# Kernel tuning notes

Hardware: AMD Instinct MI355X
Metric: run time of the kernel (lower is better)

## Reference

```python
import jax, jax.numpy as jnp
import numpy as np

B, D, H, E = 32768, 128, 512, 16

def setup_inputs() -> dict:
    key = jax.random.key(0)
    ks = jax.random.split(key, 5)
    x = jax.random.normal(ks[0], (B, 1, D), dtype=jnp.float32)
    s1 = 1.0 / float(np.sqrt(H))   # init_ uses last-dim size: w1 last dim = H
    s2 = 1.0 / float(np.sqrt(D))   # w2 last dim = D
    sg = 1.0 / float(np.sqrt(D))   # nn.Linear(D, E) default init scale
    w1 = jax.random.uniform(ks[1], (E, D, H), minval=-s1, maxval=s1, dtype=jnp.float32)
    w2 = jax.random.uniform(ks[2], (E, H, D), minval=-s2, maxval=s2, dtype=jnp.float32)
    wg = jax.random.uniform(ks[3], (D, E), minval=-sg, maxval=sg, dtype=jnp.float32)
    bg = jax.random.uniform(ks[4], (E,), minval=-sg, maxval=sg, dtype=jnp.float32)
    return {"x": x, "w1": w1, "w2": w2, "wg": wg, "bg": bg}

def reference(x, w1, w2, wg, bg):
    xt = x[:, 0, :]                                   # (B, D); seq dim is 1 by construction
    logits = xt @ wg + bg                             # (B, E)
    topk_vals, topk_idx = jax.lax.top_k(logits, 1)    # (B, 1) each
    scores = jax.nn.softmax(topk_vals, axis=-1)       # (B, 1); all ones for k=1
    # every expert processes every token (faithful to the reference)
    hidden = jax.nn.gelu(jnp.einsum('bd,edh->ebh', xt, w1), approximate=False)  # (E, B, H)
    eout = jnp.einsum('ebh,ehd->ebd', hidden, w2)     # (E, B, D)
    # gather selected expert per token, scale, sum over k
    sel = jnp.take_along_axis(eout.transpose(1, 0, 2), topk_idx[:, :, None], axis=1)  # (B, 1, D)
    return (sel * scores[:, :, None]).sum(axis=1)     # (B, D)
```

## Files before the change

kernel.cpp:

```cpp
#include <hip/hip_runtime.h>
#include <hip/hip_bf16.h>
#include <math.h>

#define NB 32768
#define DD 128
#define HH 512
#define EE 16
#define TM 32
#define HC 64
#define NCH (HH / HC)

typedef __attribute__((ext_vector_type(8))) short short8;
typedef __attribute__((ext_vector_type(4))) float f32x4;
typedef __attribute__((address_space(1))) const unsigned short gc_us;
typedef __attribute__((address_space(3))) unsigned short lds_us;

__device__ __forceinline__ unsigned short f2bf(float f) {
  union { float f; unsigned u; } v; v.f = f;
  unsigned r = v.u + 0x7fffu + ((v.u >> 16) & 1u);
  return (unsigned short)(r >> 16);
}

__device__ __forceinline__ float fast_erf(float z) {
  float a = fabsf(z);
  float t = __builtin_amdgcn_rcpf(1.0f + 0.3275911f * a);
  float y = t * (0.254829592f + t * (-0.284496736f + t * (1.421413741f +
            t * (-1.453152027f + t * 1.061405429f))));
  float r = 1.0f - y * __expf(-a * a);
  return z < 0.0f ? -r : r;
}

__global__ __launch_bounds__(256) void prep_kernel(
    const float* __restrict__ x, const float* __restrict__ wg,
    const float* __restrict__ bg, const float* __restrict__ w1,
    const float* __restrict__ w2, int* __restrict__ counts,
    int* __restrict__ rows, unsigned short* __restrict__ w1T,
    unsigned short* __restrict__ w2T) {
  __shared__ __align__(16) char smem[50816];
  int tid = threadIdx.x;

  if (blockIdx.x >= 512) {
    float (*tile)[65] = (float (*)[65])smem;
    int tp = blockIdx.x - 512;
    const float* src; unsigned short* dst; int S, Sd;
    if (tp < 256) {
      int e = tp >> 4, t2 = tp & 15;
      int d0 = (t2 >> 3) * 64, h0 = (t2 & 7) * 64;
      src = w1 + (size_t)e * DD * HH + (size_t)d0 * HH + h0; S = HH;
      dst = w1T + (size_t)e * HH * DD + (size_t)h0 * DD + d0; Sd = DD;
    } else {
      int t = tp - 256;
      int e = t >> 4, t2 = t & 15;
      int h0 = (t2 >> 1) * 64, d0 = (t2 & 1) * 64;
      src = w2 + (size_t)e * HH * DD + (size_t)h0 * DD + d0; S = DD;
      dst = w2T + (size_t)e * DD * HH + (size_t)d0 * HH + h0; Sd = HH;
    }
    #pragma unroll
    for (int i = 0; i < 4; ++i) {
      int u = tid + i * 256, r = u >> 4, c = (u & 15) * 4;
      float4 v = *(const float4*)(src + (size_t)r * S + c);
      tile[r][c + 0] = v.x; tile[r][c + 1] = v.y;
      tile[r][c + 2] = v.z; tile[r][c + 3] = v.w;
    }
    __syncthreads();
    #pragma unroll
    for (int i = 0; i < 4; ++i) {
      int u = tid + i * 256, tr = u >> 4, tc = (u & 15) * 4;
      ushort4 p;
      p.x = f2bf(tile[tc + 0][tr]); p.y = f2bf(tile[tc + 1][tr]);
      p.z = f2bf(tile[tc + 2][tr]); p.w = f2bf(tile[tc + 3][tr]);
      *(ushort4*)(dst + (size_t)tr * Sd + tc) = p;
    }
    return;
  }

  float  (*sx)[132] = (float (*)[132])smem;
  double (*swg)[EE] = (double (*)[EE])(smem + 33792);
  int* lcnt  = (int*)(smem + 50176);
  int* gbase = lcnt + EE;
  int* lslot = gbase + EE;
  int* lexp  = lslot + 64;

  int base = blockIdx.x * 64;
  if (tid < EE) lcnt[tid] = 0;
  for (int i = tid; i < DD * EE; i += 256) swg[i >> 4][i & 15] = (double)wg[i];
  {
    int r = tid >> 2, c0 = (tid & 3) * 32;
    const float4* src = (const float4*)(x + (size_t)(base + r) * DD + c0);
    #pragma unroll
    for (int i = 0; i < 8; ++i)
      *(float4*)&sx[r][c0 + i * 4] = src[i];
  }
  __syncthreads();

  int r = tid >> 2;
  int e0 = (tid & 3) * 4;
  double acc[4];
  #pragma unroll
  for (int j = 0; j < 4; ++j) acc[j] = (double)bg[e0 + j];

  #pragma unroll 4
  for (int d = 0; d < DD; ++d) {
    double xv = (double)sx[r][d];
    #pragma unroll
    for (int j = 0; j < 4; ++j)
      acc[j] += xv * swg[d][e0 + j];
  }

  int beste = 0; double bestv = acc[0];
  #pragma unroll
  for (int j = 1; j < 4; ++j)
    if (acc[j] > bestv) { bestv = acc[j]; beste = j; }
  int ge = e0 + beste;

  #pragma unroll
  for (int off = 1; off < 4; off <<= 1) {
    double ov = __shfl_xor(bestv, off);
    int oe = __shfl_xor(ge, off);
    if (ov > bestv || (ov == bestv && oe < ge)) { bestv = ov; ge = oe; }
  }

  if ((tid & 3) == 0) {
    lslot[r] = atomicAdd(&lcnt[ge], 1);
    lexp[r] = ge;
  }
  __syncthreads();
  if (tid < EE && lcnt[tid] > 0)
    gbase[tid] = atomicAdd(&counts[tid], lcnt[tid]);
  __syncthreads();
  if ((tid & 3) == 0) {
    int e2 = lexp[r];
    rows[e2 * NB + gbase[e2] + lslot[r]] = base + r;
  }
}

__global__ __launch_bounds__(256, 4) void moe_gemm(
    const float* __restrict__ x, const unsigned short* __restrict__ w1T,
    const unsigned short* __restrict__ w2T, const int* __restrict__ counts,
    const int* __restrict__ rows, float* __restrict__ out) {
  int e = blockIdx.x;
  int cnt = counts[e];
  int base = blockIdx.y * TM;
  if (base >= cnt) return;

  __shared__ __align__(16) unsigned short sW1[HC * DD];
  __shared__ __align__(16) unsigned short sW2[DD * HC];
  __shared__ __align__(16) unsigned short sH[TM * 80];

  int tid = threadIdx.x;
  int wv = tid >> 6, l = tid & 63;
  int lm = l & 15, q = l >> 4;
  int rg = wv & 1;
  int hf = wv >> 1;

  const unsigned short* w1e = w1T + (size_t)e * HH * DD;
  const unsigned short* w2e = w2T + (size_t)e * DD * HH;

  short8 xa[4];
  {
    int ridx = base + rg * 16 + lm; if (ridx >= cnt) ridx = cnt - 1;
    int grow = rows[e * NB + ridx];
    const float* xr = x + (size_t)grow * DD + q * 8;
    #pragma unroll
    for (int ks = 0; ks < 4; ++ks) {
      f32x4 v0 = *(const f32x4*)(xr + ks * 32);
      f32x4 v1 = *(const f32x4*)(xr + ks * 32 + 4);
      short8 a;
      a[0] = f2bf(v0[0]); a[1] = f2bf(v0[1]); a[2] = f2bf(v0[2]); a[3] = f2bf(v0[3]);
      a[4] = f2bf(v1[0]); a[5] = f2bf(v1[1]); a[6] = f2bf(v1[2]); a[7] = f2bf(v1[3]);
      xa[ks] = a;
    }
  }

  f32x4 acc2[8];
  #pragma unroll
  for (int n = 0; n < 8; ++n) acc2[n] = (f32x4){0.f, 0.f, 0.f, 0.f};

  for (int hc = 0; hc < NCH; ++hc) {
    {
      const unsigned short* w1c = w1e + (size_t)hc * HC * DD;
      const unsigned short* w2c = w2e + (size_t)hc * HC;
      #pragma unroll
      for (int i = 0; i < 4; ++i) {
        int r = wv * 16 + i * 4 + (l >> 4);
        const unsigned short* g = w1c + (size_t)r * DD + (((l & 15) ^ (r & 7)) << 3);
        __builtin_amdgcn_global_load_lds((gc_us*)g,
            (lds_us*)(&sW1[wv * 2048 + i * 512]), 16, 0, 0);
      }
      #pragma unroll
      for (int i = 0; i < 4; ++i) {
        int r = wv * 32 + i * 8 + (l >> 3);
        const unsigned short* g = w2c + (size_t)r * HH + (((l & 7) ^ (r & 7)) << 3);
        __builtin_amdgcn_global_load_lds((gc_us*)g,
            (lds_us*)(&sW2[wv * 2048 + i * 512]), 16, 0, 0);
      }
    }
    __syncthreads();

    f32x4 acc1[2];
    #pragma unroll
    for (int n = 0; n < 2; ++n) acc1[n] = (f32x4){0.f, 0.f, 0.f, 0.f};
    #pragma unroll
    for (int ks = 0; ks < 4; ++ks) {
      #pragma unroll
      for (int n = 0; n < 2; ++n) {
        int row = hf * 32 + n * 16 + lm;
        int sl = ((ks * 4 + q) ^ (row & 7)) * 8;
        short8 bfr = *(const short8*)&sW1[row * DD + sl];
        acc1[n] = __builtin_amdgcn_mfma_f32_16x16x32_bf16(xa[ks], bfr, acc1[n], 0, 0, 0);
      }
    }
    #pragma unroll
    for (int n = 0; n < 2; ++n) {
      #pragma unroll
      for (int rr = 0; rr < 4; ++rr) {
        float v = acc1[n][rr];
        float g = 0.5f * v * (1.0f + fast_erf(v * 0.70710678118654752f));
        sH[(rg * 16 + q * 4 + rr) * 80 + hf * 32 + n * 16 + lm] = f2bf(g);
      }
    }
    {
      short8 a = *(const short8*)&sH[(rg * 16 + lm) * 80 + hf * 32 + q * 8];
      #pragma unroll
      for (int n = 0; n < 8; ++n) {
        int row = n * 16 + lm;
        int sl = ((hf * 4 + q) ^ (row & 7)) * 8;
        short8 bfr = *(const short8*)&sW2[row * HC + sl];
        acc2[n] = __builtin_amdgcn_mfma_f32_16x16x32_bf16(a, bfr, acc2[n], 0, 0, 0);
      }
    }
    __syncthreads();
  }

  float* sc = (rg == 0) ? (float*)sW1 : (float*)sW2;
  if (hf == 1) {
    #pragma unroll
    for (int n = 0; n < 8; ++n)
      #pragma unroll
      for (int rr = 0; rr < 4; ++rr)
        sc[(q * 4 + rr) * 132 + n * 16 + lm] = acc2[n][rr];
  }
  __syncthreads();
  if (hf == 0) {
    #pragma unroll
    for (int rr = 0; rr < 4; ++rr) {
      int ml = rg * 16 + q * 4 + rr;
      int ridx = base + ml;
      if (ridx < cnt) {
        int grow = rows[e * NB + ridx];
        float* op = out + (size_t)grow * DD + lm;
        #pragma unroll
        for (int n = 0; n < 8; ++n)
          op[n * 16] = acc2[n][rr] + sc[(q * 4 + rr) * 132 + n * 16 + lm];
      }
    }
  }
}

extern "C" void kernel_launch(void* const* d_in, const int* in_sizes, int n_in,
                              void* d_out, int out_size, void* d_ws, size_t ws_size,
                              hipStream_t stream) {
  const float* x  = (const float*)d_in[0];
  const float* w1 = (const float*)d_in[1];
  const float* w2 = (const float*)d_in[2];
  const float* wg = (const float*)d_in[3];
  const float* bg = (const float*)d_in[4];
  float* out = (float*)d_out;

  int* counts = (int*)d_ws;
  int* rows   = (int*)((char*)d_ws + 1024);
  unsigned short* w1T = (unsigned short*)((char*)d_ws + 1024 + (size_t)EE * NB * 4);
  unsigned short* w2T = w1T + (size_t)EE * HH * DD;

  hipMemsetAsync(d_ws, 0, 64, stream);
  hipLaunchKernelGGL(prep_kernel, dim3(1024), dim3(256), 0, stream,
                     x, wg, bg, w1, w2, counts, rows, w1T, w2T);
  hipLaunchKernelGGL(moe_gemm, dim3(EE, NB / TM), dim3(256), 0, stream,
                     x, w1T, w2T, counts, rows, out);
}
```

Before: 129.5 us.

## Double-buffer expert weight chunks and double the row tile per block

Each block now covers 64 token rows with 512 threads, so every staged expert weight chunk is reused across twice as many rows. Weight chunks are double-buffered in LDS: the next chunk is loaded while the current one is computed, and one barrier per chunk is dropped. Half the waves stage W1 and the other half stage W2. The cost is about 73KB of LDS per block, which limits occupancy, and more padding work for experts whose token count is not a multiple of 64.

```diff
diff --git a/kernel.cpp b/kernel.cpp
--- a/kernel.cpp
+++ b/kernel.cpp
@@ -6,7 +6,7 @@
 #define DD 128
 #define HH 512
 #define EE 16
-#define TM 32
+#define TM 64
 #define HC 64
 #define NCH (HH / HC)
 
@@ -134,7 +134,7 @@
   }
 }
 
-__global__ __launch_bounds__(256, 4) void moe_gemm(
+__global__ __launch_bounds__(512, 4) void moe_gemm(
     const float* __restrict__ x, const unsigned short* __restrict__ w1T,
     const unsigned short* __restrict__ w2T, const int* __restrict__ counts,
     const int* __restrict__ rows, float* __restrict__ out) {
@@ -143,15 +143,16 @@
   int base = blockIdx.y * TM;
   if (base >= cnt) return;
 
-  __shared__ __align__(16) unsigned short sW1[HC * DD];
-  __shared__ __align__(16) unsigned short sW2[DD * HC];
-  __shared__ __align__(16) unsigned short sH[TM * 80];
+  __shared__ __align__(16) unsigned short smem[37376];
+  unsigned short* sW1 = smem;
+  unsigned short* sW2 = smem + 16384;
+  unsigned short* sH  = smem + 32768;
 
   int tid = threadIdx.x;
   int wv = tid >> 6, l = tid & 63;
   int lm = l & 15, q = l >> 4;
-  int rg = wv & 1;
-  int hf = wv >> 1;
+  int rg = wv & 3;
+  int hf = wv >> 2;
 
   const unsigned short* w1e = w1T + (size_t)e * HH * DD;
   const unsigned short* w2e = w2T + (size_t)e * DD * HH;
@@ -172,30 +173,40 @@
     }
   }
 
-  f32x4 acc2[8];
-  #pragma unroll
-  for (int n = 0; n < 8; ++n) acc2[n] = (f32x4){0.f, 0.f, 0.f, 0.f};
-
-  for (int hc = 0; hc < NCH; ++hc) {
-    {
-      const unsigned short* w1c = w1e + (size_t)hc * HC * DD;
-      const unsigned short* w2c = w2e + (size_t)hc * HC;
+  auto stage_chunk = [&](int buf, int c) {
+    if (wv < 4) {
+      const unsigned short* w1c = w1e + (size_t)c * HC * DD;
       #pragma unroll
       for (int i = 0; i < 4; ++i) {
         int r = wv * 16 + i * 4 + (l >> 4);
         const unsigned short* g = w1c + (size_t)r * DD + (((l & 15) ^ (r & 7)) << 3);
         __builtin_amdgcn_global_load_lds((gc_us*)g,
-            (lds_us*)(&sW1[wv * 2048 + i * 512]), 16, 0, 0);
-      }
+            (lds_us*)(sW1 + buf * 8192 + wv * 2048 + i * 512), 16, 0, 0);
+      }
+    } else {
+      int wz = wv - 4;
+      const unsigned short* w2c = w2e + (size_t)c * HC;
       #pragma unroll
       for (int i = 0; i < 4; ++i) {
-        int r = wv * 32 + i * 8 + (l >> 3);
+        int r = wz * 32 + i * 8 + (l >> 3);
         const unsigned short* g = w2c + (size_t)r * HH + (((l & 7) ^ (r & 7)) << 3);
         __builtin_amdgcn_global_load_lds((gc_us*)g,
-            (lds_us*)(&sW2[wv * 2048 + i * 512]), 16, 0, 0);
-      }
-    }
-    __syncthreads();
+            (lds_us*)(sW2 + buf * 8192 + wz * 2048 + i * 512), 16, 0, 0);
+      }
+    }
+  };
+
+  stage_chunk(0, 0);
+  __syncthreads();
+
+  f32x4 acc2[8];
+  #pragma unroll
+  for (int n = 0; n < 8; ++n) acc2[n] = (f32x4){0.f, 0.f, 0.f, 0.f};
+
+  for (int hc = 0; hc < NCH; ++hc) {
+    int b = hc & 1;
+
+    if (hc + 1 < NCH) stage_chunk(b ^ 1, hc + 1);
 
     f32x4 acc1[2];
     #pragma unroll
@@ -206,7 +217,7 @@
       for (int n = 0; n < 2; ++n) {
         int row = hf * 32 + n * 16 + lm;
         int sl = ((ks * 4 + q) ^ (row & 7)) * 8;
-        short8 bfr = *(const short8*)&sW1[row * DD + sl];
+        short8 bfr = *(const short8*)&sW1[b * 8192 + row * DD + sl];
         acc1[n] = __builtin_amdgcn_mfma_f32_16x16x32_bf16(xa[ks], bfr, acc1[n], 0, 0, 0);
       }
     }
@@ -216,29 +227,30 @@
       for (int rr = 0; rr < 4; ++rr) {
         float v = acc1[n][rr];
         float g = 0.5f * v * (1.0f + fast_erf(v * 0.70710678118654752f));
-        sH[(rg * 16 + q * 4 + rr) * 80 + hf * 32 + n * 16 + lm] = f2bf(g);
+        sH[(rg * 16 + q * 4 + rr) * 72 + hf * 32 + n * 16 + lm] = f2bf(g);
       }
     }
     {
-      short8 a = *(const short8*)&sH[(rg * 16 + lm) * 80 + hf * 32 + q * 8];
+      short8 a = *(const short8*)&sH[(rg * 16 + lm) * 72 + hf * 32 + q * 8];
       #pragma unroll
       for (int n = 0; n < 8; ++n) {
         int row = n * 16 + lm;
         int sl = ((hf * 4 + q) ^ (row & 7)) * 8;
-        short8 bfr = *(const short8*)&sW2[row * HC + sl];
+        short8 bfr = *(const short8*)&sW2[b * 8192 + row * HC + sl];
         acc2[n] = __builtin_amdgcn_mfma_f32_16x16x32_bf16(a, bfr, acc2[n], 0, 0, 0);
       }
     }
+
     __syncthreads();
   }
 
-  float* sc = (rg == 0) ? (float*)sW1 : (float*)sW2;
+  float* sc = (float*)smem;
   if (hf == 1) {
     #pragma unroll
     for (int n = 0; n < 8; ++n)
       #pragma unroll
       for (int rr = 0; rr < 4; ++rr)
-        sc[(q * 4 + rr) * 132 + n * 16 + lm] = acc2[n][rr];
+        sc[(rg * 16 + q * 4 + rr) * 132 + n * 16 + lm] = acc2[n][rr];
   }
   __syncthreads();
   if (hf == 0) {
@@ -251,7 +263,7 @@
         float* op = out + (size_t)grow * DD + lm;
         #pragma unroll
         for (int n = 0; n < 8; ++n)
-          op[n * 16] = acc2[n][rr] + sc[(q * 4 + rr) * 132 + n * 16 + lm];
+          op[n * 16] = acc2[n][rr] + sc[(rg * 16 + q * 4 + rr) * 132 + n * 16 + lm];
       }
     }
   }
@@ -275,6 +287,6 @@
   hipMemsetAsync(d_ws, 0, 64, stream);
   hipLaunchKernelGGL(prep_kernel, dim3(1024), dim3(256), 0, stream,
                      x, wg, bg, w1, w2, counts, rows, w1T, w2T);
-  hipLaunchKernelGGL(moe_gemm, dim3(EE, NB / TM), dim3(256), 0, stream,
+  hipLaunchKernelGGL(moe_gemm, dim3(EE, NB / TM), dim3(512), 0, stream,
                      x, w1T, w2T, counts, rows, out);
 }
```

Result: no change. 131.3 us (+1.4%).
